# Kernel tuning notes

Measured on AMD Instinct MI355X. Metric: run time of the kernel, lower is better.

The kernel has to match this reference:

```python
import jax, jax.numpy as jnp
import numpy as np
from jax import lax

QBITS = 8  # per layer_configs: 8-bit weights and activations


def fake_quant(x, bits=QBITS):
    """Per-tensor symmetric fake quantization with straight-through estimator."""
    qmax = float(2 ** (bits - 1) - 1)  # 127 for 8-bit
    scale = jnp.maximum(jnp.max(jnp.abs(x)), 1e-8) / qmax
    q = jnp.clip(jnp.round(x / scale), -qmax - 1.0, qmax) * scale
    # STE: forward uses q, backward passes gradient through unchanged
    return x + lax.stop_gradient(q - x)


def qconv(x, w, b):
    """Fake-quantized conv: quantize activations and weights, then VALID conv + bias."""
    xq = fake_quant(x)
    wq = fake_quant(w)
    y = lax.conv_general_dilated(
        xq, wq, window_strides=(1, 1), padding='VALID',
        dimension_numbers=('NCHW', 'OIHW', 'NCHW'))
    return y + b[None, :, None, None]


def setup_inputs() -> dict:
    key = jax.random.key(0)
    ks = jax.random.split(key, 9)
    return {
        'x':  jax.random.uniform(ks[0], (256, 1, 128, 128), dtype=jnp.float32),
        'w1': jax.random.normal(ks[1], (16, 1, 3, 3), dtype=jnp.float32) * 0.3,
        'b1': jax.random.normal(ks[2], (16,), dtype=jnp.float32) * 0.05,
        'w2': jax.random.normal(ks[3], (16, 16, 3, 3), dtype=jnp.float32) * 0.1,
        'b2': jax.random.normal(ks[4], (16,), dtype=jnp.float32) * 0.05,
        'w3': jax.random.normal(ks[5], (16, 16, 3, 3), dtype=jnp.float32) * 0.1,
        'b3': jax.random.normal(ks[6], (16,), dtype=jnp.float32) * 0.05,
        'w4': jax.random.normal(ks[7], (1, 16, 2, 2), dtype=jnp.float32) * 0.1,
        'b4': jax.random.normal(ks[8], (1,), dtype=jnp.float32) * 0.05,
    }


def reference(x, w1, b1, w2, b2, w3, b3, w4, b4):
    # x: [N,1,128,128] -> [N,16,126,126] -> [N,16,124,124] -> [N,16,122,122] -> [N,1,121,121]
    h = jax.nn.relu(qconv(x, w1, b1))
    h = jax.nn.relu(qconv(h, w2, b2))
    h = jax.nn.relu(qconv(h, w3, b3))
    return jax.nn.sigmoid(qconv(h, w4, b4))
```

## Files before the change

### kernel.cpp

```cpp
#include <hip/hip_runtime.h>
#include <math.h>


#define THREADS 256

typedef __attribute__((ext_vector_type(4))) int i32x4;

__device__ __forceinline__ int xcd_swz(int bid, int nwg) {
    return (bid & 7) * (nwg >> 3) + (bid >> 3);
}
__device__ __forceinline__ int swzb(int rec) {
    return (rec << 4) ^ ((rec & 56) << 1);
}

__device__ __forceinline__ float block_reduce_max(float m, float* wred) {
#pragma unroll
    for (int off = 32; off > 0; off >>= 1)
        m = fmaxf(m, __shfl_down(m, off, 64));
    if ((threadIdx.x & 63) == 0) wred[threadIdx.x >> 6] = m;
    __syncthreads();
    return fmaxf(fmaxf(wred[0], wred[1]), fmaxf(wred[2], wred[3]));
}

__global__ void init_kernel(unsigned int* slots) {
    if (threadIdx.x < 8) slots[threadIdx.x] = 0u;
}

__global__ void fill_kernel(float* out, int n, float v) {
    int i = blockIdx.x * blockDim.x + threadIdx.x;
    int stride = gridDim.x * blockDim.x;
    for (; i < n; i += stride) out[i] = v;
}

__global__ __launch_bounds__(THREADS) void absmax4_kernel(
    const float4* __restrict__ x, int n4, unsigned int* __restrict__ slot) {
    __shared__ float wred[4];
    float m = 0.f;
    const int stride = gridDim.x * blockDim.x;
    for (int i = blockIdx.x * blockDim.x + threadIdx.x; i < n4; i += stride) {
        float4 v = x[i];
        m = fmaxf(fmaxf(fabsf(v.x), fabsf(v.y)),
                  fmaxf(fmaxf(fabsf(v.z), fabsf(v.w)), m));
    }
    m = block_reduce_max(m, wred);
    if (threadIdx.x == 0) atomicMax(slot, __float_as_uint(m));
}

__global__ __launch_bounds__(THREADS) void quant_w_kernel(
    const float* __restrict__ w1, const float* __restrict__ w2,
    const float* __restrict__ w3, const float* __restrict__ w4,
    float* __restrict__ qw1, int* __restrict__ qw1p, float* __restrict__ qw4,
    signed char* __restrict__ wi8_2, signed char* __restrict__ wi8_3,
    unsigned int* __restrict__ slots) {
    __shared__ float wred[4];
    const float* w; int nel;
    switch (blockIdx.x) {
        case 0:  w = w1; nel = 144;  break;
        case 1:  w = w2; nel = 2304; break;
        case 2:  w = w3; nel = 2304; break;
        default: w = w4; nel = 64;   break;
    }
    float m = 0.f;
    for (int i = threadIdx.x; i < nel; i += blockDim.x)
        m = fmaxf(m, fabsf(w[i]));
    m = block_reduce_max(m, wred);
    if (threadIdx.x == 0) slots[4 + blockIdx.x] = __float_as_uint(m);
    const float s = fmaxf(m, 1e-8f) / 127.0f;

    if (blockIdx.x == 0) {
        for (int i = threadIdx.x; i < 144; i += blockDim.x) {
            int p = i % 9, o = i / 9;
            float q = fminf(fmaxf(rintf(w[i] / s), -128.f), 127.f);
            qw1[p * 16 + o] = q * s;
        }
        if (threadIdx.x < 64) {
            int qq = threadIdx.x >> 4, co = threadIdx.x & 15;
            unsigned pk = 0u;
            if (qq < 3) {
#pragma unroll
                for (int dx = 0; dx < 3; ++dx) {
                    float qv = fminf(fmaxf(rintf(w[co * 9 + qq * 3 + dx] / s),
                                           -128.f), 127.f);
                    pk |= ((unsigned)(int)qv & 0xffu) << (8 * dx);
                }
            }
            qw1p[threadIdx.x] = (int)pk;
        }
    } else if (blockIdx.x == 3) {
        for (int i = threadIdx.x; i < 64; i += blockDim.x) {
            float q = fminf(fmaxf(rintf(w[i] / s), -128.f), 127.f);
            qw4[i] = q * s;
        }
    } else {
        signed char* wi8 = (blockIdx.x == 1) ? wi8_2 : wi8_3;
        for (int i = threadIdx.x; i < 3072; i += blockDim.x) {
            int ci = i & 15, lane = (i >> 4) & 63, g = i >> 10;
            int co = lane & 15, qq = lane >> 4;
            int pos = 4 * g + qq;
            float v = 0.f;
            if (pos < 9) {
                int ky = pos / 3, kx = pos % 3;
                v = fminf(fmaxf(rintf(w[((co * 16 + ci) * 3 + ky) * 3 + kx] / s),
                                -128.f), 127.f);
            }
            wi8[i] = (signed char)(int)v;
        }
    }
}

__global__ __launch_bounds__(THREADS) void conv1max_kernel(
    const float* __restrict__ x, const float* __restrict__ qw,
    const float* __restrict__ bias, unsigned int* __restrict__ slots) {
    constexpr int IH = 128, IW = 128, OH = 126, OW = 126;
    __shared__ float tile[34 * 34];
    __shared__ float wred[4];
    const int bid = xcd_swz(blockIdx.x, gridDim.x);
    const int n = bid >> 4, tr = bid & 15;
    const int oy0 = (tr >> 2) * 32, ox0 = (tr & 3) * 32;
    const float s_in = fmaxf(__uint_as_float(slots[0]), 1e-8f) / 127.0f;
    const float* xN = x + (size_t)n * IH * IW;

#pragma unroll
    for (int it = 0; it < 5; ++it) {
        int px = it * 256 + threadIdx.x;
        if (px < 1156) {
            int iy = px / 34, ix = px - iy * 34;
            int gy = min(oy0 + iy, IH - 1), gx = min(ox0 + ix, IW - 1);
            float q = rintf(xN[gy * IW + gx] / s_in);
            tile[px] = fminf(fmaxf(q, -128.f), 127.f);
        }
    }
    __syncthreads();

    const int tx = (threadIdx.x & 15) * 2, ty = (threadIdx.x >> 4) * 2;
    float p[4][4];
#pragma unroll
    for (int r = 0; r < 4; ++r) {
        const float* rp = &tile[(ty + r) * 34 + tx];
        p[r][0] = rp[0]; p[r][1] = rp[1]; p[r][2] = rp[2]; p[r][3] = rp[3];
    }
    float accm[16];
#pragma unroll
    for (int c = 0; c < 16; ++c) accm[c] = -3.0e38f;

#pragma unroll
    for (int sy = 0; sy < 2; ++sy)
#pragma unroll
    for (int sx = 0; sx < 2; ++sx) {
        float acc[16];
#pragma unroll
        for (int c = 0; c < 16; ++c) acc[c] = 0.f;
#pragma unroll
        for (int ky = 0; ky < 3; ++ky)
#pragma unroll
        for (int kx = 0; kx < 3; ++kx) {
            const float xv = p[sy + ky][sx + kx];
            const float* wp = qw + (ky * 3 + kx) * 16;
#pragma unroll
            for (int co = 0; co < 16; ++co)
                acc[co] = fmaf(xv, wp[co], acc[co]);
        }
        const int oy = oy0 + ty + sy, ox = ox0 + tx + sx;
        if (oy < OH && ox < OW) {
#pragma unroll
            for (int co = 0; co < 16; ++co)
                accm[co] = fmaxf(accm[co], acc[co]);
        }
    }
    float m = 0.f;
#pragma unroll
    for (int co = 0; co < 16; ++co)
        m = fmaxf(m, fmaxf(fmaf(accm[co], s_in, bias[co]), 0.f));
    m = block_reduce_max(m, wred);
    if (threadIdx.x == 0) atomicMax(&slots[1], __float_as_uint(m));
}

__global__ __launch_bounds__(THREADS) void k3_kernel(
    const float* __restrict__ x, const int* __restrict__ qw1p,
    const float* __restrict__ b1, signed char* __restrict__ h1out,
    const signed char* __restrict__ wi8_2, const float* __restrict__ b2,
    unsigned int* __restrict__ slots) {
    __shared__ signed char xq[40 * 40];
    __shared__ signed char h1t[34 * 34 * 16 + 128];
    __shared__ float wred[4];
    const int bid = xcd_swz(blockIdx.x, gridDim.x);
    const int n = bid >> 4, tr = bid & 15;
    const int ty = (tr >> 2) * 32, tx = (tr & 3) * 32;
    const int tid = threadIdx.x, lane = tid & 63, wv = tid >> 6;
    const int q = lane >> 4, col = lane & 15;

    const float s_x  = fmaxf(__uint_as_float(slots[0]), 1e-8f) / 127.0f;
    const float sw1  = fmaxf(__uint_as_float(slots[4]), 1e-8f) / 127.0f;
    const float sxw1 = s_x * sw1;
    const float r1   = 127.0f / fmaxf(__uint_as_float(slots[1]), 1e-8f);
    const float* xN = x + (size_t)n * 128 * 128;

    for (int i = tid; i < 1296; i += THREADS) {
        int iy = i / 36, ix = i - iy * 36;
        int gy = min(ty + iy, 127), gx = min(tx + ix, 127);
        float qf = rintf(xN[gy * 128 + gx] / s_x);
        qf = fminf(fmaxf(qf, -128.f), 127.f);
        xq[iy * 40 + ix] = (signed char)(int)qf;
    }

    i32x4 a1 = {qw1p[q * 16 + col], 0, 0, 0};
    i32x4 af2[3];
#pragma unroll
    for (int g = 0; g < 3; ++g)
        af2[g] = ((const i32x4*)wi8_2)[g * 64 + lane];
    float b1j[4], b2j[4];
#pragma unroll
    for (int j = 0; j < 4; ++j) { b1j[j] = b1[q * 4 + j]; b2j[j] = b2[q * 4 + j]; }
    __syncthreads();

    for (int py = wv; py < 34; py += 4) {
#pragma unroll
        for (int g3 = 0; g3 < 3; ++g3) {
            const int pxx = g3 * 16 + col;
            const int base = (py + q) * 40 + (pxx & ~3);
            unsigned lo = *(const unsigned*)(xq + base);
            unsigned hi = *(const unsigned*)(xq + base + 4);
            unsigned win = (unsigned)((((unsigned long long)hi << 32) | lo)
                                      >> ((pxx & 3) * 8));
            i32x4 b = {(int)win, 0, 0, 0};
            i32x4 z = {0, 0, 0, 0};
            i32x4 acc = __builtin_amdgcn_mfma_i32_16x16x64_i8(a1, b, z, 0, 0, 0);
            if (pxx < 34) {
                unsigned pk = 0u;
#pragma unroll
                for (int j = 0; j < 4; ++j) {
                    float y = fmaxf(fmaf((float)acc[j], sxw1, b1j[j]), 0.f);
                    float q8 = fminf(rintf(y * r1), 127.f);
                    pk |= ((unsigned)(int)q8) << (j * 8);
                }
                *(unsigned*)(h1t + swzb(py * 34 + pxx) + q * 4) = pk;
                const int gy = ty + py, gx = tx + pxx;
                if (gy <= 125 && gx <= 125)
                    *(unsigned*)(h1out + ((size_t)(n * 126 + gy) * 126 + gx) * 16
                                 + q * 4) = pk;
            }
        }
    }
    __syncthreads();

    const int wr = wv >> 1, wc = wv & 1;
    int drec[3];
#pragma unroll
    for (int g = 0; g < 3; ++g) {
        int pos = 4 * g + q;
        int dy = (pos < 9) ? pos / 3 : 0;
        int dx = (pos < 9) ? pos % 3 : 0;
        drec[g] = dy * 34 + dx;
    }
    const int ix2 = 16 * wc + col;
    int mi[4];
#pragma unroll
    for (int j = 0; j < 4; ++j) mi[j] = INT_MIN;

#pragma unroll 4
    for (int r = 0; r < 16; ++r) {
        const int iy2 = 16 * wr + r;
        const int rec = iy2 * 34 + ix2;
        i32x4 acc = {0, 0, 0, 0};
#pragma unroll
        for (int g = 0; g < 3; ++g) {
            i32x4 b = *(const i32x4*)(h1t + swzb(rec + drec[g]));
            acc = __builtin_amdgcn_mfma_i32_16x16x64_i8(af2[g], b, acc, 0, 0, 0);
        }
        if (ty + iy2 <= 123 && tx + ix2 <= 123) {
#pragma unroll
            for (int j = 0; j < 4; ++j)
                mi[j] = (acc[j] > mi[j]) ? acc[j] : mi[j];
        }
    }
    const float s1  = fmaxf(__uint_as_float(slots[1]), 1e-8f) / 127.0f;
    const float sw2 = fmaxf(__uint_as_float(slots[5]), 1e-8f) / 127.0f;
    const float sxw = s1 * sw2;
    float m = 0.f;
#pragma unroll
    for (int j = 0; j < 4; ++j)
        m = fmaxf(m, fmaxf(fmaf((float)mi[j], sxw, b2j[j]), 0.f));
    m = block_reduce_max(m, wred);
    if (tid == 0) atomicMax(&slots[2], __float_as_uint(m));
}

__global__ __launch_bounds__(THREADS) void k4_kernel(
    const signed char* __restrict__ h1, const signed char* __restrict__ wi8_2,
    const float* __restrict__ b2, signed char* __restrict__ h2out,
    const signed char* __restrict__ wi8_3, const float* __restrict__ b3,
    unsigned int* __restrict__ slots) {
    __shared__ signed char h1t[34 * 34 * 16 + 128];
    __shared__ signed char h2t[32 * 32 * 16 + 128];
    __shared__ float wred[4];
    const int bid = xcd_swz(blockIdx.x, gridDim.x);
    const int n = bid / 25, tr = bid % 25;
    const int ty = (tr / 5) * 30, tx = (tr % 5) * 30;
    const int tid = threadIdx.x, lane = tid & 63, wv = tid >> 6;
    const int q = lane >> 4, col = lane & 15;
    const int wr = wv >> 1, wc = wv & 1;

    const signed char* h1N = h1 + (size_t)n * 126 * 126 * 16;
#pragma unroll
    for (int it = 0; it < 5; ++it) {
        int p = it * 256 + tid;
        if (p < 1156) {
            int iy = p / 34, ix = p - iy * 34;
            int gy = min(ty + iy, 125), gx = min(tx + ix, 125);
            *(int4*)(h1t + swzb(p)) =
                *(const int4*)(h1N + ((size_t)gy * 126 + gx) * 16);
        }
    }
    i32x4 af2[3], af3[3];
#pragma unroll
    for (int g = 0; g < 3; ++g) {
        af2[g] = ((const i32x4*)wi8_2)[g * 64 + lane];
        af3[g] = ((const i32x4*)wi8_3)[g * 64 + lane];
    }
    __syncthreads();

    int d34[3], d32[3];
#pragma unroll
    for (int g = 0; g < 3; ++g) {
        int pos = 4 * g + q;
        int dy = (pos < 9) ? pos / 3 : 0;
        int dx = (pos < 9) ? pos % 3 : 0;
        d34[g] = dy * 34 + dx;
        d32[g] = dy * 32 + dx;
    }
    const float s1  = fmaxf(__uint_as_float(slots[1]), 1e-8f) / 127.0f;
    const float sw2 = fmaxf(__uint_as_float(slots[5]), 1e-8f) / 127.0f;
    const float sxw2 = s1 * sw2;
    const float r2 = 127.0f / fmaxf(__uint_as_float(slots[2]), 1e-8f);
    float b2j[4];
#pragma unroll
    for (int j = 0; j < 4; ++j) b2j[j] = b2[q * 4 + j];

    const int ix2 = 16 * wc + col;
    signed char* h2N = h2out + (size_t)n * 124 * 124 * 16;

#pragma unroll 4
    for (int r = 0; r < 16; ++r) {
        const int iy2 = 16 * wr + r;
        const int rec = iy2 * 34 + ix2;
        i32x4 acc = {0, 0, 0, 0};
#pragma unroll
        for (int g = 0; g < 3; ++g) {
            i32x4 b = *(const i32x4*)(h1t + swzb(rec + d34[g]));
            acc = __builtin_amdgcn_mfma_i32_16x16x64_i8(af2[g], b, acc, 0, 0, 0);
        }
        unsigned pk = 0u;
#pragma unroll
        for (int j = 0; j < 4; ++j) {
            float y = fmaxf(fmaf((float)acc[j], sxw2, b2j[j]), 0.f);
            float q8 = fminf(rintf(y * r2), 127.f);
            pk |= ((unsigned)(int)q8) << (j * 8);
        }
        *(unsigned*)(h2t + swzb(iy2 * 32 + ix2) + q * 4) = pk;
        const int gy = ty + iy2, gx = tx + ix2;
        if (gy <= 123 && gx <= 123)
            *(unsigned*)(h2N + ((size_t)gy * 124 + gx) * 16 + q * 4) = pk;
    }
    __syncthreads();

    int mi[4];
#pragma unroll
    for (int j = 0; j < 4; ++j) mi[j] = INT_MIN;
#pragma unroll 4
    for (int r = 0; r < 16; ++r) {
        const int iy3 = 16 * wr + r;
        if (iy3 <= 29) {
            const int rec = iy3 * 32 + ix2;
            i32x4 acc = {0, 0, 0, 0};
#pragma unroll
            for (int g = 0; g < 3; ++g) {
                i32x4 b = *(const i32x4*)(h2t + swzb(rec + d32[g]));
                acc = __builtin_amdgcn_mfma_i32_16x16x64_i8(af3[g], b, acc, 0, 0, 0);
            }
            if (ix2 <= 29 && ty + iy3 <= 121 && tx + ix2 <= 121) {
#pragma unroll
                for (int j = 0; j < 4; ++j)
                    mi[j] = (acc[j] > mi[j]) ? acc[j] : mi[j];
            }
        }
    }
    const float s2  = fmaxf(__uint_as_float(slots[2]), 1e-8f) / 127.0f;
    const float sw3 = fmaxf(__uint_as_float(slots[6]), 1e-8f) / 127.0f;
    const float sxw3 = s2 * sw3;
    float m = 0.f;
#pragma unroll
    for (int j = 0; j < 4; ++j)
        m = fmaxf(m, fmaxf(fmaf((float)mi[j], sxw3, b3[q * 4 + j]), 0.f));
    m = block_reduce_max(m, wred);
    if (tid == 0) atomicMax(&slots[3], __float_as_uint(m));
}

__global__ __launch_bounds__(THREADS) void k5_kernel(
    const signed char* __restrict__ h2, const signed char* __restrict__ wi8_3,
    const float* __restrict__ b3, const float* __restrict__ qw4,
    const float* __restrict__ b4, float* __restrict__ out,
    unsigned int* __restrict__ slots) {
    __shared__ signed char h2t[34 * 34 * 16 + 128];
    __shared__ signed char h3t[32 * 32 * 16 + 128];
    const int bid = xcd_swz(blockIdx.x, gridDim.x);
    const int n = bid / 25, tr = bid % 25;
    const int ty = (tr / 5) * 30, tx = (tr % 5) * 30;
    const int tid = threadIdx.x, lane = tid & 63, wv = tid >> 6;
    const int q = lane >> 4, col = lane & 15;
    const int wr = wv >> 1, wc = wv & 1;

    const signed char* h2N = h2 + (size_t)n * 124 * 124 * 16;
#pragma unroll
    for (int it = 0; it < 5; ++it) {
        int p = it * 256 + tid;
        if (p < 1156) {
            int iy = p / 34, ix = p - iy * 34;
            int gy = min(ty + iy, 123), gx = min(tx + ix, 123);
            *(int4*)(h2t + swzb(p)) =
                *(const int4*)(h2N + ((size_t)gy * 124 + gx) * 16);
        }
    }
    i32x4 af3[3];
#pragma unroll
    for (int g = 0; g < 3; ++g)
        af3[g] = ((const i32x4*)wi8_3)[g * 64 + lane];
    __syncthreads();

    int d34[3];
#pragma unroll
    for (int g = 0; g < 3; ++g) {
        int pos = 4 * g + q;
        int dy = (pos < 9) ? pos / 3 : 0;
        int dx = (pos < 9) ? pos % 3 : 0;
        d34[g] = dy * 34 + dx;
    }
    const float s2  = fmaxf(__uint_as_float(slots[2]), 1e-8f) / 127.0f;
    const float sw3 = fmaxf(__uint_as_float(slots[6]), 1e-8f) / 127.0f;
    const float sxw3 = s2 * sw3;
    const float r3 = 127.0f / fmaxf(__uint_as_float(slots[3]), 1e-8f);
    float b3j[4];
#pragma unroll
    for (int j = 0; j < 4; ++j) b3j[j] = b3[q * 4 + j];
    const int ix3 = 16 * wc + col;

#pragma unroll 4
    for (int r = 0; r < 16; ++r) {
        const int iy3 = 16 * wr + r;
        const int rec = iy3 * 34 + ix3;
        i32x4 acc = {0, 0, 0, 0};
#pragma unroll
        for (int g = 0; g < 3; ++g) {
            i32x4 b = *(const i32x4*)(h2t + swzb(rec + d34[g]));
            acc = __builtin_amdgcn_mfma_i32_16x16x64_i8(af3[g], b, acc, 0, 0, 0);
        }
        unsigned pk = 0u;
#pragma unroll
        for (int j = 0; j < 4; ++j) {
            float y = fmaxf(fmaf((float)acc[j], sxw3, b3j[j]), 0.f);
            float q8 = fminf(rintf(y * r3), 127.f);
            pk |= ((unsigned)(int)q8) << (j * 8);
        }
        *(unsigned*)(h3t + swzb(iy3 * 32 + ix3) + q * 4) = pk;
    }
    __syncthreads();

    const float s3 = fmaxf(__uint_as_float(slots[3]), 1e-8f) / 127.0f;
    const float bb = b4[0];
    float w[64];
#pragma unroll
    for (int i = 0; i < 64; ++i) w[i] = qw4[i];
    float* outN = out + (size_t)n * 121 * 121;

#pragma unroll
    for (int it = 0; it < 4; ++it) {
        int p = it * 256 + tid;
        if (p < 961) {
            int r = p / 31, c = p - r * 31;
            float acc = 0.f;
#pragma unroll
            for (int ky = 0; ky < 2; ++ky)
#pragma unroll
            for (int kx = 0; kx < 2; ++kx) {
                union { int4 v; signed char ch[16]; } u;
                u.v = *(const int4*)(h3t + swzb((r + ky) * 32 + (c + kx)));
#pragma unroll
                for (int ci = 0; ci < 16; ++ci)
                    acc = fmaf((float)u.ch[ci], w[(ci * 2 + ky) * 2 + kx], acc);
            }
            const int gy = ty + r, gx = tx + c;
            if (gy <= 120 && gx <= 120) {
                float y = fmaf(acc, s3, bb);
                outN[(size_t)gy * 121 + gx] = 1.0f / (1.0f + expf(-y));
            }
        }
    }
}

extern "C" void kernel_launch(void* const* d_in, const int* in_sizes, int n_in,
                              void* d_out, int out_size, void* d_ws, size_t ws_size,
                              hipStream_t stream) {
    (void)in_sizes; (void)n_in;
    const float* x  = (const float*)d_in[0];
    const float* w1 = (const float*)d_in[1];
    const float* b1 = (const float*)d_in[2];
    const float* w2 = (const float*)d_in[3];
    const float* b2 = (const float*)d_in[4];
    const float* w3 = (const float*)d_in[5];
    const float* b3 = (const float*)d_in[6];
    const float* w4 = (const float*)d_in[7];
    const float* b4 = (const float*)d_in[8];

    char* ws = (char*)d_ws;
    unsigned int* slots = (unsigned int*)ws;
    float* qw1 = (float*)(ws + 256);
    int*   qw1p = (int*)(ws + 1024);
    float* qw4 = (float*)(ws + 1536);
    signed char* wi8_2 = (signed char*)(ws + 2048);
    signed char* wi8_3 = (signed char*)(ws + 5120);

    const size_t Q1 = 65028096ULL;
    const size_t Q2 = 62980096ULL;
    signed char* qb1 = (signed char*)(ws + 32768);
    signed char* qb2 = (signed char*)(ws + 32768 + Q1);
    float* outp = (float*)d_out;

    const size_t need = 32768ULL + Q1 + Q2;
    if (ws_size < need) {
        float v = 100.0f + (float)(ws_size >> 20);
        hipLaunchKernelGGL(fill_kernel, dim3(1024), dim3(THREADS), 0, stream,
                           outp, out_size, v);
        return;
    }

    hipLaunchKernelGGL(init_kernel, dim3(1), dim3(64), 0, stream, slots);
    hipLaunchKernelGGL(absmax4_kernel, dim3(2048), dim3(THREADS), 0, stream,
                       (const float4*)x, 256 * 128 * 128 / 4, slots + 0);
    hipLaunchKernelGGL(quant_w_kernel, dim3(4), dim3(THREADS), 0, stream,
                       w1, w2, w3, w4, qw1, qw1p, qw4, wi8_2, wi8_3, slots);

    hipLaunchKernelGGL(conv1max_kernel, dim3(256 * 16), dim3(THREADS), 0, stream,
                       x, qw1, b1, slots);
    hipLaunchKernelGGL(k3_kernel, dim3(256 * 16), dim3(THREADS), 0, stream,
                       x, qw1p, b1, qb1, wi8_2, b2, slots);
    const int fgrid = 256 * 25;
    hipLaunchKernelGGL(k4_kernel, dim3(fgrid), dim3(THREADS), 0, stream,
                       qb1, wi8_2, b2, qb2, wi8_3, b3, slots);
    hipLaunchKernelGGL(k5_kernel, dim3(fgrid), dim3(THREADS), 0, stream,
                       qb2, wi8_3, b3, qw4, b4, outp, slots);
}
```

Measured before the change: 311.1 us.

## Move conv1 absmax pass and final 2x2 conv onto int8 MFMA, fold requant scales

Rewrites the conv1 max-scan kernel to quantize x to int8 in shared memory and compute the 16-channel 3x3 conv with an int8 MFMA using the packed layer-1 weights, as k3 already does, replacing the fp32 FMA loop. The final 2x2 conv in k5 likewise becomes one int8 MFMA per 16-pixel segment, using a new pre-packed int8 w4 layout, instead of a per-thread scalar dot product. Requantization folds scale and reciprocal into a single fma plus clamp, and the per-row bounds checks are hoisted into precomputed flags. Integer accumulation is exact, but the MFMA output in k5 wastes three of its four row groups.

```diff
diff --git a/kernel.cpp b/kernel.cpp
--- a/kernel.cpp
+++ b/kernel.cpp
@@ -1,5 +1,6 @@
 #include <hip/hip_runtime.h>
 #include <math.h>
+#include <limits.h>
 
 
 #define THREADS 256
@@ -49,8 +50,8 @@
 __global__ __launch_bounds__(THREADS) void quant_w_kernel(
     const float* __restrict__ w1, const float* __restrict__ w2,
     const float* __restrict__ w3, const float* __restrict__ w4,
-    float* __restrict__ qw1, int* __restrict__ qw1p, float* __restrict__ qw4,
-    signed char* __restrict__ wi8_2, signed char* __restrict__ wi8_3,
+    int* __restrict__ qw1p, signed char* __restrict__ wi8_2,
+    signed char* __restrict__ wi8_3, signed char* __restrict__ wi8_4,
     unsigned int* __restrict__ slots) {
     __shared__ float wred[4];
     const float* w; int nel;
@@ -68,11 +69,6 @@
     const float s = fmaxf(m, 1e-8f) / 127.0f;
 
     if (blockIdx.x == 0) {
-        for (int i = threadIdx.x; i < 144; i += blockDim.x) {
-            int p = i % 9, o = i / 9;
-            float q = fminf(fmaxf(rintf(w[i] / s), -128.f), 127.f);
-            qw1[p * 16 + o] = q * s;
-        }
         if (threadIdx.x < 64) {
             int qq = threadIdx.x >> 4, co = threadIdx.x & 15;
             unsigned pk = 0u;
@@ -87,9 +83,12 @@
             qw1p[threadIdx.x] = (int)pk;
         }
     } else if (blockIdx.x == 3) {
-        for (int i = threadIdx.x; i < 64; i += blockDim.x) {
-            float q = fminf(fmaxf(rintf(w[i] / s), -128.f), 127.f);
-            qw4[i] = q * s;
+        for (int i = threadIdx.x; i < 1024; i += blockDim.x) {
+            int ci = i & 15, lane = (i >> 4) & 63;
+            int tap = lane >> 4, ky = tap >> 1, kx = tap & 1;
+            float v = fminf(fmaxf(rintf(w[(ci * 2 + ky) * 2 + kx] / s),
+                                  -128.f), 127.f);
+            wi8_4[i] = (signed char)(int)v;
         }
     } else {
         signed char* wi8 = (blockIdx.x == 1) ? wi8_2 : wi8_3;
@@ -108,71 +107,65 @@
     }
 }
 
-__global__ __launch_bounds__(THREADS) void conv1max_kernel(
-    const float* __restrict__ x, const float* __restrict__ qw,
-    const float* __restrict__ bias, unsigned int* __restrict__ slots) {
-    constexpr int IH = 128, IW = 128, OH = 126, OW = 126;
-    __shared__ float tile[34 * 34];
+__global__ __launch_bounds__(THREADS) void c1max_kernel(
+    const float* __restrict__ x, const int* __restrict__ qw1p,
+    const float* __restrict__ b1, unsigned int* __restrict__ slots) {
+    __shared__ signed char xq[40 * 40];
     __shared__ float wred[4];
     const int bid = xcd_swz(blockIdx.x, gridDim.x);
     const int n = bid >> 4, tr = bid & 15;
-    const int oy0 = (tr >> 2) * 32, ox0 = (tr & 3) * 32;
-    const float s_in = fmaxf(__uint_as_float(slots[0]), 1e-8f) / 127.0f;
-    const float* xN = x + (size_t)n * IH * IW;
-
-#pragma unroll
-    for (int it = 0; it < 5; ++it) {
-        int px = it * 256 + threadIdx.x;
-        if (px < 1156) {
-            int iy = px / 34, ix = px - iy * 34;
-            int gy = min(oy0 + iy, IH - 1), gx = min(ox0 + ix, IW - 1);
-            float q = rintf(xN[gy * IW + gx] / s_in);
-            tile[px] = fminf(fmaxf(q, -128.f), 127.f);
-        }
-    }
-    __syncthreads();
-
-    const int tx = (threadIdx.x & 15) * 2, ty = (threadIdx.x >> 4) * 2;
-    float p[4][4];
-#pragma unroll
-    for (int r = 0; r < 4; ++r) {
-        const float* rp = &tile[(ty + r) * 34 + tx];
-        p[r][0] = rp[0]; p[r][1] = rp[1]; p[r][2] = rp[2]; p[r][3] = rp[3];
-    }
-    float accm[16];
-#pragma unroll
-    for (int c = 0; c < 16; ++c) accm[c] = -3.0e38f;
-
-#pragma unroll
-    for (int sy = 0; sy < 2; ++sy)
-#pragma unroll
-    for (int sx = 0; sx < 2; ++sx) {
-        float acc[16];
-#pragma unroll
-        for (int c = 0; c < 16; ++c) acc[c] = 0.f;
-#pragma unroll
-        for (int ky = 0; ky < 3; ++ky)
-#pragma unroll
-        for (int kx = 0; kx < 3; ++kx) {
-            const float xv = p[sy + ky][sx + kx];
-            const float* wp = qw + (ky * 3 + kx) * 16;
-#pragma unroll
-            for (int co = 0; co < 16; ++co)
-                acc[co] = fmaf(xv, wp[co], acc[co]);
-        }
-        const int oy = oy0 + ty + sy, ox = ox0 + tx + sx;
-        if (oy < OH && ox < OW) {
-#pragma unroll
-            for (int co = 0; co < 16; ++co)
-                accm[co] = fmaxf(accm[co], acc[co]);
+    const int ty = (tr >> 2) * 32, tx = (tr & 3) * 32;
+    const int tid = threadIdx.x, lane = tid & 63, wv = tid >> 6;
+    const int q = lane >> 4, col = lane & 15;
+
+    const float s_x = fmaxf(__uint_as_float(slots[0]), 1e-8f) / 127.0f;
+    const float sw1 = fmaxf(__uint_as_float(slots[4]), 1e-8f) / 127.0f;
+    const float sxw1 = s_x * sw1;
+    const float* xN = x + (size_t)n * 128 * 128;
+
+    for (int i = tid; i < 1296; i += THREADS) {
+        int iy = i / 36, ix = i - iy * 36;
+        int gy = min(ty + iy, 127), gx = min(tx + ix, 127);
+        float qf = rintf(xN[gy * 128 + gx] / s_x);
+        qf = fminf(fmaxf(qf, -128.f), 127.f);
+        xq[iy * 40 + ix] = (signed char)(int)qf;
+    }
+    i32x4 a1 = {qw1p[q * 16 + col], 0, 0, 0};
+    __syncthreads();
+
+    bool okx[3];
+#pragma unroll
+    for (int g3 = 0; g3 < 3; ++g3) {
+        int pxx = g3 * 16 + col;
+        okx[g3] = (pxx < 34) && (tx + pxx <= 125);
+    }
+    int mi[4] = {INT_MIN, INT_MIN, INT_MIN, INT_MIN};
+    for (int py = wv; py < 34; py += 4) {
+        const bool oky = (ty + py <= 125);
+#pragma unroll
+        for (int g3 = 0; g3 < 3; ++g3) {
+            const int pxx = g3 * 16 + col;
+            const int base = (py + q) * 40 + (pxx & ~3);
+            unsigned lo = *(const unsigned*)(xq + base);
+            unsigned hi = *(const unsigned*)(xq + base + 4);
+            unsigned win = (unsigned)((((unsigned long long)hi << 32) | lo)
+                                      >> ((pxx & 3) * 8));
+            i32x4 b = {(int)win, 0, 0, 0};
+            i32x4 z = {0, 0, 0, 0};
+            i32x4 acc = __builtin_amdgcn_mfma_i32_16x16x64_i8(a1, b, z, 0, 0, 0);
+            if (oky && okx[g3]) {
+#pragma unroll
+                for (int j = 0; j < 4; ++j)
+                    mi[j] = (acc[j] > mi[j]) ? acc[j] : mi[j];
+            }
         }
     }
     float m = 0.f;
 #pragma unroll
-    for (int co = 0; co < 16; ++co)
-        m = fmaxf(m, fmaxf(fmaf(accm[co], s_in, bias[co]), 0.f));
+    for (int j = 0; j < 4; ++j)
+        m = fmaxf(m, fmaxf(fmaf((float)mi[j], sxw1, b1[q * 4 + j]), 0.f));
     m = block_reduce_max(m, wred);
-    if (threadIdx.x == 0) atomicMax(&slots[1], __float_as_uint(m));
+    if (tid == 0) atomicMax(&slots[1], __float_as_uint(m));
 }
 
 __global__ __launch_bounds__(THREADS) void k3_kernel(
@@ -191,8 +184,8 @@
 
     const float s_x  = fmaxf(__uint_as_float(slots[0]), 1e-8f) / 127.0f;
     const float sw1  = fmaxf(__uint_as_float(slots[4]), 1e-8f) / 127.0f;
-    const float sxw1 = s_x * sw1;
     const float r1   = 127.0f / fmaxf(__uint_as_float(slots[1]), 1e-8f);
+    const float A1   = (s_x * sw1) * r1;
     const float* xN = x + (size_t)n * 128 * 128;
 
     for (int i = tid; i < 1296; i += THREADS) {
@@ -208,12 +201,22 @@
 #pragma unroll
     for (int g = 0; g < 3; ++g)
         af2[g] = ((const i32x4*)wi8_2)[g * 64 + lane];
-    float b1j[4], b2j[4];
-#pragma unroll
-    for (int j = 0; j < 4; ++j) { b1j[j] = b1[q * 4 + j]; b2j[j] = b2[q * 4 + j]; }
-    __syncthreads();
-
+    float B1j[4], b2j[4];
+#pragma unroll
+    for (int j = 0; j < 4; ++j) {
+        B1j[j] = b1[q * 4 + j] * r1;
+        b2j[j] = b2[q * 4 + j];
+    }
+    __syncthreads();
+
+    bool okx[3];
+#pragma unroll
+    for (int g3 = 0; g3 < 3; ++g3) {
+        int pxx = g3 * 16 + col;
+        okx[g3] = (pxx < 34) && (tx + pxx <= 125);
+    }
     for (int py = wv; py < 34; py += 4) {
+        const bool oky = (ty + py <= 125);
 #pragma unroll
         for (int g3 = 0; g3 < 3; ++g3) {
             const int pxx = g3 * 16 + col;
@@ -229,15 +232,15 @@
                 unsigned pk = 0u;
 #pragma unroll
                 for (int j = 0; j < 4; ++j) {
-                    float y = fmaxf(fmaf((float)acc[j], sxw1, b1j[j]), 0.f);
-                    float q8 = fminf(rintf(y * r1), 127.f);
+                    float t = fmaf((float)acc[j], A1, B1j[j]);
+                    float q8 = fminf(fmaxf(rintf(t), 0.f), 127.f);
                     pk |= ((unsigned)(int)q8) << (j * 8);
                 }
                 *(unsigned*)(h1t + swzb(py * 34 + pxx) + q * 4) = pk;
-                const int gy = ty + py, gx = tx + pxx;
-                if (gy <= 125 && gx <= 125)
-                    *(unsigned*)(h1out + ((size_t)(n * 126 + gy) * 126 + gx) * 16
-                                 + q * 4) = pk;
+                if (oky && okx[g3])
+                    *(unsigned*)(h1out +
+                        ((size_t)(n * 126 + ty + py) * 126 + tx + pxx) * 16
+                        + q * 4) = pk;
             }
         }
     }
@@ -253,21 +256,20 @@
         drec[g] = dy * 34 + dx;
     }
     const int ix2 = 16 * wc + col;
-    int mi[4];
-#pragma unroll
-    for (int j = 0; j < 4; ++j) mi[j] = INT_MIN;
+    const bool okc = (tx + ix2 <= 123);
+    const int rlim2 = 123 - ty - 16 * wr;
+    int mi[4] = {INT_MIN, INT_MIN, INT_MIN, INT_MIN};
 
 #pragma unroll 4
     for (int r = 0; r < 16; ++r) {
-        const int iy2 = 16 * wr + r;
-        const int rec = iy2 * 34 + ix2;
+        const int rec = (16 * wr + r) * 34 + ix2;
         i32x4 acc = {0, 0, 0, 0};
 #pragma unroll
         for (int g = 0; g < 3; ++g) {
             i32x4 b = *(const i32x4*)(h1t + swzb(rec + drec[g]));
             acc = __builtin_amdgcn_mfma_i32_16x16x64_i8(af2[g], b, acc, 0, 0, 0);
         }
-        if (ty + iy2 <= 123 && tx + ix2 <= 123) {
+        if (okc && r <= rlim2) {
 #pragma unroll
             for (int j = 0; j < 4; ++j)
                 mi[j] = (acc[j] > mi[j]) ? acc[j] : mi[j];
@@ -329,14 +331,20 @@
     }
     const float s1  = fmaxf(__uint_as_float(slots[1]), 1e-8f) / 127.0f;
     const float sw2 = fmaxf(__uint_as_float(slots[5]), 1e-8f) / 127.0f;
-    const float sxw2 = s1 * sw2;
-    const float r2 = 127.0f / fmaxf(__uint_as_float(slots[2]), 1e-8f);
-    float b2j[4];
-#pragma unroll
-    for (int j = 0; j < 4; ++j) b2j[j] = b2[q * 4 + j];
+    const float r2  = 127.0f / fmaxf(__uint_as_float(slots[2]), 1e-8f);
+    const float A2  = (s1 * sw2) * r2;
+    float B2j[4], b3j[4];
+#pragma unroll
+    for (int j = 0; j < 4; ++j) {
+        B2j[j] = b2[q * 4 + j] * r2;
+        b3j[j] = b3[q * 4 + j];
+    }
 
     const int ix2 = 16 * wc + col;
     signed char* h2N = h2out + (size_t)n * 124 * 124 * 16;
+    const bool gxok = (tx + ix2 <= 123);
+    const int rlim = 123 - ty - 16 * wr;
+    int goff = ((ty + 16 * wr) * 124 + tx + ix2) * 16 + q * 4;
 
 #pragma unroll 4
     for (int r = 0; r < 16; ++r) {
@@ -351,20 +359,20 @@
         unsigned pk = 0u;
 #pragma unroll
         for (int j = 0; j < 4; ++j) {
-            float y = fmaxf(fmaf((float)acc[j], sxw2, b2j[j]), 0.f);
-            float q8 = fminf(rintf(y * r2), 127.f);
+            float t = fmaf((float)acc[j], A2, B2j[j]);
+            float q8 = fminf(fmaxf(rintf(t), 0.f), 127.f);
             pk |= ((unsigned)(int)q8) << (j * 8);
         }
         *(unsigned*)(h2t + swzb(iy2 * 32 + ix2) + q * 4) = pk;
-        const int gy = ty + iy2, gx = tx + ix2;
-        if (gy <= 123 && gx <= 123)
-            *(unsigned*)(h2N + ((size_t)gy * 124 + gx) * 16 + q * 4) = pk;
-    }
-    __syncthreads();
-
-    int mi[4];
-#pragma unroll
-    for (int j = 0; j < 4; ++j) mi[j] = INT_MIN;
+        if (gxok && r <= rlim)
+            *(unsigned*)(h2N + goff) = pk;
+        goff += 124 * 16;
+    }
+    __syncthreads();
+
+    const bool okc3 = (ix2 <= 29) && (tx + ix2 <= 121);
+    const int rlim3 = min(29, 121 - ty) - 16 * wr;
+    int mi[4] = {INT_MIN, INT_MIN, INT_MIN, INT_MIN};
 #pragma unroll 4
     for (int r = 0; r < 16; ++r) {
         const int iy3 = 16 * wr + r;
@@ -376,7 +384,7 @@
                 i32x4 b = *(const i32x4*)(h2t + swzb(rec + d32[g]));
                 acc = __builtin_amdgcn_mfma_i32_16x16x64_i8(af3[g], b, acc, 0, 0, 0);
             }
-            if (ix2 <= 29 && ty + iy3 <= 121 && tx + ix2 <= 121) {
+            if (okc3 && r <= rlim3) {
 #pragma unroll
                 for (int j = 0; j < 4; ++j)
                     mi[j] = (acc[j] > mi[j]) ? acc[j] : mi[j];
@@ -389,14 +397,14 @@
     float m = 0.f;
 #pragma unroll
     for (int j = 0; j < 4; ++j)
-        m = fmaxf(m, fmaxf(fmaf((float)mi[j], sxw3, b3[q * 4 + j]), 0.f));
+        m = fmaxf(m, fmaxf(fmaf((float)mi[j], sxw3, b3j[j]), 0.f));
     m = block_reduce_max(m, wred);
     if (tid == 0) atomicMax(&slots[3], __float_as_uint(m));
 }
 
 __global__ __launch_bounds__(THREADS) void k5_kernel(
     const signed char* __restrict__ h2, const signed char* __restrict__ wi8_3,
-    const float* __restrict__ b3, const float* __restrict__ qw4,
+    const float* __restrict__ b3, const signed char* __restrict__ wi8_4,
     const float* __restrict__ b4, float* __restrict__ out,
     unsigned int* __restrict__ slots) {
     __shared__ signed char h2t[34 * 34 * 16 + 128];
@@ -423,6 +431,7 @@
 #pragma unroll
     for (int g = 0; g < 3; ++g)
         af3[g] = ((const i32x4*)wi8_3)[g * 64 + lane];
+    i32x4 a4 = ((const i32x4*)wi8_4)[lane];
     __syncthreads();
 
     int d34[3];
@@ -435,11 +444,11 @@
     }
     const float s2  = fmaxf(__uint_as_float(slots[2]), 1e-8f) / 127.0f;
     const float sw3 = fmaxf(__uint_as_float(slots[6]), 1e-8f) / 127.0f;
-    const float sxw3 = s2 * sw3;
-    const float r3 = 127.0f / fmaxf(__uint_as_float(slots[3]), 1e-8f);
-    float b3j[4];
-#pragma unroll
-    for (int j = 0; j < 4; ++j) b3j[j] = b3[q * 4 + j];
+    const float r3  = 127.0f / fmaxf(__uint_as_float(slots[3]), 1e-8f);
+    const float A3  = (s2 * sw3) * r3;
+    float B3j[4];
+#pragma unroll
+    for (int j = 0; j < 4; ++j) B3j[j] = b3[q * 4 + j] * r3;
     const int ix3 = 16 * wc + col;
 
 #pragma unroll 4
@@ -455,41 +464,33 @@
         unsigned pk = 0u;
 #pragma unroll
         for (int j = 0; j < 4; ++j) {
-            float y = fmaxf(fmaf((float)acc[j], sxw3, b3j[j]), 0.f);
-            float q8 = fminf(rintf(y * r3), 127.f);
+            float t = fmaf((float)acc[j], A3, B3j[j]);
+            float q8 = fminf(fmaxf(rintf(t), 0.f), 127.f);
             pk |= ((unsigned)(int)q8) << (j * 8);
         }
         *(unsigned*)(h3t + swzb(iy3 * 32 + ix3) + q * 4) = pk;
     }
     __syncthreads();
 
-    const float s3 = fmaxf(__uint_as_float(slots[3]), 1e-8f) / 127.0f;
-    const float bb = b4[0];
-    float w[64];
-#pragma unroll
-    for (int i = 0; i < 64; ++i) w[i] = qw4[i];
+    const float s3  = fmaxf(__uint_as_float(slots[3]), 1e-8f) / 127.0f;
+    const float sw4 = fmaxf(__uint_as_float(slots[7]), 1e-8f) / 127.0f;
+    const float sy4 = s3 * sw4;
+    const float b40 = b4[0];
+    const int ky4 = q >> 1, kx4 = q & 1;
     float* outN = out + (size_t)n * 121 * 121;
 
-#pragma unroll
-    for (int it = 0; it < 4; ++it) {
-        int p = it * 256 + tid;
-        if (p < 961) {
-            int r = p / 31, c = p - r * 31;
-            float acc = 0.f;
-#pragma unroll
-            for (int ky = 0; ky < 2; ++ky)
-#pragma unroll
-            for (int kx = 0; kx < 2; ++kx) {
-                union { int4 v; signed char ch[16]; } u;
-                u.v = *(const int4*)(h3t + swzb((r + ky) * 32 + (c + kx)));
-#pragma unroll
-                for (int ci = 0; ci < 16; ++ci)
-                    acc = fmaf((float)u.ch[ci], w[(ci * 2 + ky) * 2 + kx], acc);
-            }
-            const int gy = ty + r, gx = tx + c;
-            if (gy <= 120 && gx <= 120) {
-                float y = fmaf(acc, s3, bb);
-                outN[(size_t)gy * 121 + gx] = 1.0f / (1.0f + expf(-y));
+    for (int r = wv; r < 31; r += 4) {
+#pragma unroll
+        for (int seg = 0; seg < 2; ++seg) {
+            const int c = seg * 16 + col;
+            const int rec = (r + ky4) * 32 + c + kx4;
+            i32x4 b = *(const i32x4*)(h3t + swzb(rec));
+            i32x4 z = {0, 0, 0, 0};
+            i32x4 acc = __builtin_amdgcn_mfma_i32_16x16x64_i8(a4, b, z, 0, 0, 0);
+            if (q == 0 && c <= 30 && ty + r <= 120 && tx + c <= 120) {
+                float yv = fmaf((float)acc[0], sy4, b40);
+                outN[(size_t)(ty + r) * 121 + tx + c] =
+                    1.0f / (1.0f + expf(-yv));
             }
         }
     }
@@ -511,11 +512,10 @@
 
     char* ws = (char*)d_ws;
     unsigned int* slots = (unsigned int*)ws;
-    float* qw1 = (float*)(ws + 256);
-    int*   qw1p = (int*)(ws + 1024);
-    float* qw4 = (float*)(ws + 1536);
+    int* qw1p = (int*)(ws + 256);
     signed char* wi8_2 = (signed char*)(ws + 2048);
     signed char* wi8_3 = (signed char*)(ws + 5120);
+    signed char* wi8_4 = (signed char*)(ws + 8192);
 
     const size_t Q1 = 65028096ULL;
     const size_t Q2 = 62980096ULL;
@@ -535,15 +535,15 @@
     hipLaunchKernelGGL(absmax4_kernel, dim3(2048), dim3(THREADS), 0, stream,
                        (const float4*)x, 256 * 128 * 128 / 4, slots + 0);
     hipLaunchKernelGGL(quant_w_kernel, dim3(4), dim3(THREADS), 0, stream,
-                       w1, w2, w3, w4, qw1, qw1p, qw4, wi8_2, wi8_3, slots);
-
-    hipLaunchKernelGGL(conv1max_kernel, dim3(256 * 16), dim3(THREADS), 0, stream,
-                       x, qw1, b1, slots);
+                       w1, w2, w3, w4, qw1p, wi8_2, wi8_3, wi8_4, slots);
+
+    hipLaunchKernelGGL(c1max_kernel, dim3(256 * 16), dim3(THREADS), 0, stream,
+                       x, qw1p, b1, slots);
     hipLaunchKernelGGL(k3_kernel, dim3(256 * 16), dim3(THREADS), 0, stream,
                        x, qw1p, b1, qb1, wi8_2, b2, slots);
     const int fgrid = 256 * 25;
     hipLaunchKernelGGL(k4_kernel, dim3(fgrid), dim3(THREADS), 0, stream,
                        qb1, wi8_2, b2, qb2, wi8_3, b3, slots);
     hipLaunchKernelGGL(k5_kernel, dim3(fgrid), dim3(THREADS), 0, stream,
-                       qb2, wi8_3, b3, qw4, b4, outp, slots);
-}
+                       qb2, wi8_3, b3, wi8_4, b4, outp, slots);
+}
```

After: 317.0 us. No clear change (+1.9%).
